# Optimization experiments

Measured on AMD Instinct MI355X. Metric: run time of the kernel, lower is better.

## Reference

```python
import jax, jax.numpy as jnp
import numpy as np

# Dimensions: B batches, E links, T time steps, F flows, rank-r factors, K unrolled iters
B, E, T, F = 16, 256, 4096, 512
RANK = 10
NUM_ITER = 5


def setup_inputs() -> dict:
    key = jax.random.key(0)
    ks = jax.random.split(key, 9)
    Y = jax.random.normal(ks[0], (B, E, T), dtype=jnp.float32)
    R = (jax.random.uniform(ks[1], (B, E, F)) < 0.1).astype(jnp.float32)
    Omega = (jax.random.uniform(ks[2], (B, E, T)) < 0.9).astype(jnp.float32)
    P0 = jax.random.normal(ks[3], (B, E, RANK), dtype=jnp.float32) * 0.1
    Q0 = jax.random.normal(ks[4], (B, T, RANK), dtype=jnp.float32) * 0.1
    # per-iteration learned log-parameters of the unrolled network
    lam_log = jax.random.normal(ks[5], (NUM_ITER,), dtype=jnp.float32) * 0.1 - 1.0
    mu_log = jax.random.normal(ks[6], (NUM_ITER,), dtype=jnp.float32) * 0.1 - 1.0
    nu_log = jax.random.normal(ks[7], (NUM_ITER,), dtype=jnp.float32) * 0.1
    gamma_logit = jax.random.normal(ks[8], (NUM_ITER,), dtype=jnp.float32) * 0.1
    return {"Y": Y, "R": R, "Omega": Omega, "P0": P0, "Q0": Q0,
            "lam_log": lam_log, "mu_log": mu_log, "nu_log": nu_log,
            "gamma_logit": gamma_logit}


def reference(Y, R, Omega, P0, Q0, lam_log, mu_log, nu_log, gamma_logit):
    """Unrolled BSCA: Y ~ X + R @ A + noise on observed entries (Omega mask),
    X relaxed low-rank via factors P (B,E,r), Q (B,T,r); A sparse anomalies (B,F,T).
    Each iteration: rank-r ridge solves for P and Q (left=False -> rhs @ inv(lhs)),
    relaxed X update, soft-thresholded BSCA direction for A + convex-combination step."""
    rank = P0.shape[-1]
    eye = jnp.eye(rank, dtype=Y.dtype)
    X = Omega * Y                     # (B,E,T) init relaxed variable
    A = jnp.zeros((*Y.shape[:-2], R.shape[-1], Y.shape[-1]), dtype=Y.dtype)  # (B,F,T)
    P, Q = P0, Q0
    A_scale = (R * R).mT @ (Omega * Omega)          # (B,F,T)
    noobs = A_scale == 0
    A_scale_safe = A_scale + noobs.astype(Y.dtype)
    for k in range(NUM_ITER):
        lam = jnp.exp(lam_log[k])
        mu = jnp.exp(mu_log[k])
        nu = jnp.exp(nu_log[k])
        gamma = jax.nn.sigmoid(gamma_logit[k])
        regp = lam / nu
        # P update: P = (X @ Q) @ inv(Q^T Q + regp I)   (right solve; lhs symmetric)
        lhsQ = Q.mT @ Q + regp * eye                 # (B,r,r)
        P = jnp.linalg.solve(lhsQ, (X @ Q).mT).mT    # (B,E,r)
        # Q update: Q = (X^T @ P) @ inv(P^T P + regp I)
        lhsP = P.mT @ P + regp * eye
        Q = jnp.linalg.solve(lhsP, (X.mT @ P).mT).mT # (B,T,r)
        # X update (relaxed): X = (Omega*err + nu*P Q^T) / (Omega^2 + nu)
        RA = R @ A                                   # (B,E,T)
        err = Omega * (Y - RA)
        X = (Omega * err + nu * (P @ Q.mT)) / (Omega * Omega + nu)
        # A update: soft-thresholded best-response + convex combination step
        resid = Omega * (Y - X - RA)                 # (B,E,T)
        BA = A + (R.mT @ resid) / A_scale_safe       # (B,F,T)
        A_dir = jnp.sign(BA) * jnp.maximum(jnp.abs(BA) - mu / A_scale_safe, 0.0)
        A_dir = jnp.where(noobs, 0.0, A_dir)
        A = A + gamma * (A_dir - A)
    return A
```

## Files before the change

kernel.cpp:

```cpp
#include <hip/hip_runtime.h>
#include <stdint.h>

#define BB 16
#define EE 256
#define TT 4096
#define FF 512
#define RK 10
#define NIT 5

typedef short bf16x8 __attribute__((ext_vector_type(8)));
typedef float f32x4  __attribute__((ext_vector_type(4)));

__device__ __forceinline__ unsigned short f2bf(float x){
  unsigned int u = __float_as_uint(x);
  unsigned int r = (u + 0x7FFFu + ((u >> 16) & 1u)) >> 16;
  return (unsigned short)r;
}
__device__ __forceinline__ float bf2f(unsigned short s){
  return __uint_as_float(((unsigned int)s) << 16);
}

__device__ __forceinline__ void gld16(const void* g, void* l){
  __builtin_amdgcn_global_load_lds((const __attribute__((address_space(1))) unsigned int*)g,
                                   (__attribute__((address_space(3))) unsigned int*)l,
                                   16, 0, 0);
}

__device__ __forceinline__ int ssw(int r, int s){
  return ((s ^ (r & 3) ^ ((r >> 2) & 3)) << 3);
}


__global__ void k_params(const float* lam_log, const float* mu_log,
                         const float* nu_log, const float* gl, float* prm){
  int k = threadIdx.x;
  if (k < NIT){
    float lam = expf(lam_log[k]);
    float mu  = expf(mu_log[k]);
    float nu  = expf(nu_log[k]);
    float gam = 1.0f/(1.0f+expf(-gl[k]));
    prm[k*8+0]=lam; prm[k*8+1]=mu; prm[k*8+2]=nu; prm[k*8+3]=gam; prm[k*8+4]=lam/nu;
  }
}

__global__ void k_initX(const float4* __restrict__ Y, const float4* __restrict__ Om,
                        float4* __restrict__ X, ushort4* __restrict__ Omb){
  int i = blockIdx.x*256 + threadIdx.x;
  float4 y = Y[i], o = Om[i];
  X[i] = make_float4(y.x*o.x, y.y*o.y, y.z*o.z, y.w*o.w);
  ushort4 ob; ob.x=f2bf(o.x); ob.y=f2bf(o.y); ob.z=f2bf(o.z); ob.w=f2bf(o.w);
  Omb[i] = ob;
}

__global__ void k_ombit(const float* __restrict__ Om, unsigned int* __restrict__ Ombit){
  int tid = threadIdx.x;
  int wv = tid >> 6, lane = tid & 63;
  size_t base = (size_t)blockIdx.x*8192 + (size_t)wv*2048;
  for (int it=0; it<32; ++it){
    float om = Om[base + it*64 + lane];
    unsigned long long m = __ballot(om != 0.0f);
    if (lane==0)  Ombit[(base>>5) + it*2]     = (unsigned int)m;
    if (lane==32) Ombit[(base>>5) + it*2 + 1] = (unsigned int)(m>>32);
  }
}

__global__ void k_qtrans(const float* __restrict__ Q0, float* __restrict__ Qt){
  int idx = blockIdx.x*256 + threadIdx.x;
  int b = idx >> 12, t = idx & (TT-1);
  #pragma unroll
  for (int j=0;j<RK;j++)
    Qt[((size_t)b*RK + j)*TT + t] = Q0[(size_t)idx*RK + j];
}

__global__ void k_rbf(const float4* __restrict__ R, ushort4* __restrict__ Rb){
  int i = blockIdx.x*256 + threadIdx.x;
  float4 v = R[i];
  ushort4 o; o.x=f2bf(v.x); o.y=f2bf(v.y); o.z=f2bf(v.z); o.w=f2bf(v.w);
  Rb[i] = o;
}

__global__ void k_rtransb(const float* __restrict__ Rm, unsigned short* __restrict__ Rbt){
  int f = blockIdx.x, b = blockIdx.y, e = threadIdx.x;
  Rbt[((size_t)b*FF + f)*EE + e] = f2bf(Rm[((size_t)b*EE + e)*FF + f]);
}

__global__ void k_omtrans(const unsigned short* __restrict__ Omb,
                          unsigned short* __restrict__ OmbT){
  __shared__ unsigned short sT[64][66];
  int b  = blockIdx.z;
  int E0 = blockIdx.y*64, T0 = blockIdx.x*64;
  int tid = threadIdx.x;
  int fi = tid >> 4;
  int m  = tid & 15;
  #pragma unroll
  for (int pass=0; pass<4; ++pass){
    int e = pass*16 + fi;
    ushort4 v = *(const ushort4*)(Omb + ((size_t)(b*EE + E0 + e))*TT + T0 + m*4);
    sT[e][m*4+0]=v.x; sT[e][m*4+1]=v.y; sT[e][m*4+2]=v.z; sT[e][m*4+3]=v.w;
  }
  __syncthreads();
  #pragma unroll
  for (int pass=0; pass<4; ++pass){
    int t  = pass*16 + fi;
    int e4 = m*4;
    ushort4 o;
    o.x = sT[e4+0][t]; o.y = sT[e4+1][t];
    o.z = sT[e4+2][t]; o.w = sT[e4+3][t];
    *(ushort4*)(OmbT + ((size_t)b*TT + T0 + t)*EE + E0 + e4) = o;
  }
}


__global__ void k_lhsQ(const float* __restrict__ Qt, const float* __restrict__ prm,
                       float* __restrict__ lhs, int k){
  int p = blockIdx.x, b = blockIdx.y;
  int i = 0, rem = p;
  while (rem >= i+1){ rem -= (i+1); ++i; }
  int j = rem;
  const float* qi = Qt + ((size_t)b*RK + i)*TT;
  const float* qj = Qt + ((size_t)b*RK + j)*TT;
  float a = 0.0f;
  for (int t = threadIdx.x*4; t < TT; t += 1024){
    float4 x = *(const float4*)(qi+t);
    float4 y = *(const float4*)(qj+t);
    a += x.x*y.x + x.y*y.y + x.z*y.z + x.w*y.w;
  }
  __shared__ float red[256];
  red[threadIdx.x] = a; __syncthreads();
  for (int s=128; s>0; s>>=1){
    if (threadIdx.x < s) red[threadIdx.x] += red[threadIdx.x+s];
    __syncthreads();
  }
  if (threadIdx.x==0){
    float v = red[0];
    if (i==j) v += prm[k*8+4];
    lhs[(b*RK+i)*RK + j] = v;
    lhs[(b*RK+j)*RK + i] = v;
  }
}

__global__ void k_lhsP(const float* __restrict__ P, const float* __restrict__ prm,
                       float* __restrict__ lhs, int k){
  int p = blockIdx.x, b = blockIdx.y;
  int i = 0, rem = p;
  while (rem >= i+1){ rem -= (i+1); ++i; }
  int j = rem;
  int e = threadIdx.x;
  const float* pr = P + ((size_t)b*EE + e)*RK;
  float a = pr[i]*pr[j];
  __shared__ float red[256];
  red[threadIdx.x] = a; __syncthreads();
  for (int s=128; s>0; s>>=1){
    if (threadIdx.x < s) red[threadIdx.x] += red[threadIdx.x+s];
    __syncthreads();
  }
  if (threadIdx.x==0){
    float v = red[0];
    if (i==j) v += prm[k*8+4];
    lhs[(b*RK+i)*RK + j] = v;
    lhs[(b*RK+j)*RK + i] = v;
  }
}

__global__ void k_invert(const float* __restrict__ lhs, float* __restrict__ inv){
  int b = blockIdx.x;
  __shared__ float aug[RK][2*RK];
  int tid = threadIdx.x;
  int i = tid / (2*RK), j = tid % (2*RK);
  bool act = tid < RK*2*RK;
  if (act) aug[i][j] = (j < RK) ? lhs[(b*RK+i)*RK + j] : ((j-RK)==i ? 1.0f : 0.0f);
  __syncthreads();
  for (int kk=0; kk<RK; ++kk){
    float pinv = 1.0f / aug[kk][kk];
    __syncthreads();
    if (act && i==kk) aug[i][j] *= pinv;
    __syncthreads();
    float factor = (act && i!=kk) ? aug[i][kk] : 0.0f;
    float pivrow = act ? aug[kk][j] : 0.0f;
    __syncthreads();
    if (act && i!=kk) aug[i][j] -= factor * pivrow;
    __syncthreads();
  }
  if (act && j >= RK) inv[(b*RK+i)*RK + (j-RK)] = aug[i][j];
}

__global__ void k_Pupd(const float* __restrict__ X, const float* __restrict__ Qt,
                       const float* __restrict__ inv, float* __restrict__ P){
  int e = blockIdx.x, b = blockIdx.y;
  const float* xr = X + ((size_t)b*EE + e)*TT;
  const float* qb = Qt + (size_t)b*RK*TT;
  float acc[RK];
  #pragma unroll
  for (int j=0;j<RK;j++) acc[j]=0.0f;
  for (int t = threadIdx.x*4; t < TT; t += 1024){
    float4 x = *(const float4*)(xr+t);
    #pragma unroll
    for (int j=0;j<RK;j++){
      float4 q = *(const float4*)(qb + (size_t)j*TT + t);
      acc[j] += x.x*q.x + x.y*q.y + x.z*q.z + x.w*q.w;
    }
  }
  __shared__ float partial[4][RK];
  int lane = threadIdx.x & 63, wv = threadIdx.x >> 6;
  #pragma unroll
  for (int j=0;j<RK;j++){
    float v = acc[j];
    for (int s=32;s>0;s>>=1) v += __shfl_down(v, s, 64);
    if (lane==0) partial[wv][j] = v;
  }
  __syncthreads();
  if (threadIdx.x < RK){
    int i = threadIdx.x;
    float out = 0.0f;
    #pragma unroll
    for (int j=0;j<RK;j++){
      float xq = partial[0][j]+partial[1][j]+partial[2][j]+partial[3][j];
      out += xq * inv[(b*RK+j)*RK + i];
    }
    P[((size_t)b*EE + e)*RK + i] = out;
  }
}

__global__ void k_Qupd(const float* __restrict__ X, const float* __restrict__ P,
                       const float* __restrict__ inv, float* __restrict__ Qt){
  int b = blockIdx.y;
  int t = blockIdx.x*256 + threadIdx.x;
  __shared__ float sP[EE*RK];
  __shared__ float sInv[RK*RK];
  for (int i=threadIdx.x; i<EE*RK; i+=256) sP[i] = P[(size_t)b*EE*RK + i];
  if (threadIdx.x < RK*RK) sInv[threadIdx.x] = inv[b*RK*RK + threadIdx.x];
  __syncthreads();
  float acc[RK];
  #pragma unroll
  for (int j=0;j<RK;j++) acc[j]=0.0f;
  const float* xb = X + (size_t)b*EE*TT + t;
  for (int e=0;e<EE;e++){
    float x = xb[(size_t)e*TT];
    #pragma unroll
    for (int j=0;j<RK;j++) acc[j] += x * sP[e*RK+j];
  }
  #pragma unroll
  for (int i=0;i<RK;i++){
    float q = 0.0f;
    #pragma unroll
    for (int j=0;j<RK;j++) q += acc[j]*sInv[j*RK+i];
    Qt[((size_t)b*RK + i)*TT + t] = q;
  }
}

__global__ __launch_bounds__(256) void k_gemm1m(
    const unsigned short* __restrict__ Abt, const unsigned short* __restrict__ Rb,
    const float* __restrict__ Y, const unsigned int* __restrict__ Ombit,
    const float* __restrict__ Qt, const float* __restrict__ P,
    const float* __restrict__ prm, float* __restrict__ X,
    unsigned short* __restrict__ residT, int k)
{
  __shared__ __align__(16) unsigned char lds[20480];
  int id = blockIdx.x;
  int b  = id >> 7;
  int e0 = ((id >> 6) & 1) * 128;
  int t0 = (id & 63) * 64;
  int tid  = threadIdx.x;
  int lane = tid & 63, wid = tid >> 6;
  int lr = lane & 15, lg = lane >> 4;
  int wm = wid >> 1, wn = wid & 1;

  f32x4 acc[2][4];
  #pragma unroll
  for (int m=0;m<2;++m)
    #pragma unroll
    for (int n=0;n<4;++n)
      #pragma unroll
      for (int i=0;i<4;++i) acc[m][n][i]=0.0f;

  if (k > 0){
    int swz  = ((lg ^ (lr & 3) ^ ((lr >> 2) & 3)) << 4);
    int aoff = (wm*32 + lr)*64 + swz;
    int boff = 4096 + (wn*64 + lr)*64 + swz;
    int rA = tid >> 2, sA = tid & 3;
    int c0 = tid, c1 = tid + 256;
    int rB0 = c0 >> 2, sB0 = c0 & 3;
    int rB1 = c1 >> 2, sB1 = c1 & 3;
    const unsigned short* gA  = Abt + ((size_t)b*TT + t0 + rA)*FF + ssw(rA,sA);
    const unsigned short* gB0 = Rb  + ((size_t)(b*EE + e0 + rB0))*FF + ssw(rB0,sB0);
    const unsigned short* gB1 = Rb  + ((size_t)(b*EE + e0 + rB1))*FF + ssw(rB1,sB1);
    unsigned char* lA  = lds + tid*16;
    unsigned char* lB0 = lds + 4096 + c0*16;
    unsigned char* lB1 = lds + 4096 + c1*16;

    for (int kk=0; kk<16; ++kk){
      __syncthreads();
      int f0k = kk*32;
      gld16(gA  + f0k, lA);
      gld16(gB0 + f0k, lB0);
      gld16(gB1 + f0k, lB1);
      asm volatile("s_waitcnt vmcnt(0)" ::: "memory");
      __syncthreads();
      bf16x8 af[2], bb[4];
      #pragma unroll
      for (int m=0;m<2;++m) af[m] = *(const bf16x8*)(lds + aoff + m*1024);
      #pragma unroll
      for (int n=0;n<4;++n) bb[n] = *(const bf16x8*)(lds + boff + n*1024);
      #pragma unroll
      for (int m=0;m<2;++m)
        #pragma unroll
        for (int n=0;n<4;++n)
          acc[m][n] = __builtin_amdgcn_mfma_f32_16x16x32_bf16(af[m], bb[n], acc[m][n], 0, 0, 0);
    }
  }

  __syncthreads();
  unsigned short* wbuf = (unsigned short*)(lds + wid*2176);
  float* Pl = (float*)(lds + 12288);
  float* Ql = (float*)(lds + 12288 + 5120);
  for (int idx = tid; idx < 128*RK; idx += 256)
    Pl[idx] = P[((size_t)(b*EE + e0))*RK + idx];
  for (int idx = tid; idx < RK*64; idx += 256){
    int j = idx >> 6, t = idx & 63;
    Ql[idx] = Qt[((size_t)(b*RK + j))*TT + t0 + t];
  }
  __syncthreads();

  float nu = prm[k*8+2];
  #pragma unroll
  for (int m=0;m<2;++m){
    int tq = wm*32 + m*16 + lg*4;
    float4 ql4[RK];
    #pragma unroll
    for (int j=0;j<RK;++j) ql4[j] = *(const float4*)(Ql + j*64 + tq);
    asm volatile("" ::: "memory");
    #pragma unroll
    for (int n=0;n<4;++n){
      int eloc = wn*64 + n*16 + lr;
      const float* pr = Pl + eloc*RK;
      float4 pq = {0,0,0,0};
      #pragma unroll
      for (int j=0;j<RK;++j){
        float pj = pr[j];
        pq.x += pj*ql4[j].x; pq.y += pj*ql4[j].y;
        pq.z += pj*ql4[j].z; pq.w += pj*ql4[j].w;
      }
      f32x4 ra = acc[m][n];
      size_t off = ((size_t)(b*EE + e0 + eloc))*TT + t0 + tq;
      float4 y = *(const float4*)(Y + off);
      unsigned int w = Ombit[off >> 5];
      int sh = (int)(off & 31);
      float4 xo; float rs0, rs1, rs2, rs3;
      {
        float om2 = (w>>(sh+0))&1 ? 1.0f : 0.0f; float d = y.x - ra[0];
        xo.x = (om2*d + nu*pq.x)/(om2 + nu); rs0 = om2*(y.x - xo.x - ra[0]);
      }{
        float om2 = (w>>(sh+1))&1 ? 1.0f : 0.0f; float d = y.y - ra[1];
        xo.y = (om2*d + nu*pq.y)/(om2 + nu); rs1 = om2*(y.y - xo.y - ra[1]);
      }{
        float om2 = (w>>(sh+2))&1 ? 1.0f : 0.0f; float d = y.z - ra[2];
        xo.z = (om2*d + nu*pq.z)/(om2 + nu); rs2 = om2*(y.z - xo.z - ra[2]);
      }{
        float om2 = (w>>(sh+3))&1 ? 1.0f : 0.0f; float d = y.w - ra[3];
        xo.w = (om2*d + nu*pq.w)/(om2 + nu); rs3 = om2*(y.w - xo.w - ra[3]);
      }
      *(float4*)(X + off) = xo;
      int wc = n*16 + lr;
      wbuf[(lg*4+0)*68 + wc] = f2bf(rs0);
      wbuf[(lg*4+1)*68 + wc] = f2bf(rs1);
      wbuf[(lg*4+2)*68 + wc] = f2bf(rs2);
      wbuf[(lg*4+3)*68 + wc] = f2bf(rs3);
    }
    asm volatile("" ::: "memory");
    #pragma unroll
    for (int j2=0;j2<4;++j2){
      int row = j2*4 + lg;
      int c4  = lr*4;
      ushort4 vv = *(const ushort4*)(wbuf + row*68 + c4);
      *(ushort4*)(residT + ((size_t)b*TT + t0 + wm*32 + m*16 + row)*EE + e0 + wn*64 + c4) = vv;
    }
    asm volatile("" ::: "memory");
  }
}

__device__ __forceinline__ float aupd(float a, float g, unsigned short asu,
                                      float mu, float gamma){
  float as = bf2f(asu);
  bool no = (as == 0.0f);
  float rs = 1.0f / (no ? 1.0f : as);
  float ba = a + g*rs;
  float ad = copysignf(fmaxf(fabsf(ba) - mu*rs, 0.0f), ba);
  if (no) ad = 0.0f;
  return a + gamma*(ad - a);
}

__global__ __launch_bounds__(256) void k_gemm2m(
    const unsigned short* __restrict__ residT, const unsigned short* __restrict__ Rbt,
    const unsigned short* __restrict__ As, const float* __restrict__ prm,
    float* __restrict__ A, unsigned short* __restrict__ Abt, int k)
{
  __shared__ __align__(16) unsigned char lds[12288];
  int id = blockIdx.x;
  int b  = id >> 8;
  int f0 = ((id >> 5) & 7) * 64;
  int t0 = (id & 31) * 128;
  int tid  = threadIdx.x;
  int lane = tid & 63, wid = tid >> 6;
  int lr = lane & 15, lg = lane >> 4;
  int wm = wid >> 1, wn = wid & 1;

  f32x4 acc[4][2];
  #pragma unroll
  for (int m=0;m<4;++m)
    #pragma unroll
    for (int n=0;n<2;++n)
      #pragma unroll
      for (int i=0;i<4;++i) acc[m][n][i]=0.0f;

  int swz  = ((lg ^ (lr & 3) ^ ((lr >> 2) & 3)) << 4);
  int aoff = (wm*64 + lr)*64 + swz;
  int boff = 8192 + (wn*32 + lr)*64 + swz;
  int c0 = tid, c1 = tid + 256;
  int r0 = c0 >> 2, s0 = c0 & 3;
  int r1 = c1 >> 2, s1 = c1 & 3;
  int rB = tid >> 2, sB = tid & 3;
  const unsigned short* gA0 = residT + ((size_t)b*TT + t0 + r0)*EE + ssw(r0,s0);
  const unsigned short* gA1 = residT + ((size_t)b*TT + t0 + r1)*EE + ssw(r1,s1);
  const unsigned short* gB  = Rbt    + ((size_t)(b*FF + f0 + rB))*EE + ssw(rB,sB);
  unsigned char* lA0 = lds + c0*16;
  unsigned char* lA1 = lds + c1*16;
  unsigned char* lB  = lds + 8192 + tid*16;

  for (int kk=0; kk<8; ++kk){
    __syncthreads();
    int eoff = kk*32;
    gld16(gA0 + eoff, lA0);
    gld16(gA1 + eoff, lA1);
    gld16(gB  + eoff, lB);
    asm volatile("s_waitcnt vmcnt(0)" ::: "memory");
    __syncthreads();
    bf16x8 af[4], bb[2];
    #pragma unroll
    for (int m=0;m<4;++m) af[m] = *(const bf16x8*)(lds + aoff + m*1024);
    #pragma unroll
    for (int n=0;n<2;++n) bb[n] = *(const bf16x8*)(lds + boff + n*1024);
    #pragma unroll
    for (int m=0;m<4;++m)
      #pragma unroll
      for (int n=0;n<2;++n)
        acc[m][n] = __builtin_amdgcn_mfma_f32_16x16x32_bf16(af[m], bb[n], acc[m][n], 0, 0, 0);
  }

  __syncthreads();
  unsigned short* wbuf = (unsigned short*)(lds + wid*1152);
  float mu = prm[k*8+1], gamma = prm[k*8+3];
  bool emit = (k < NIT-1);
  #pragma unroll
  for (int m=0;m<4;++m){
    int tq = wm*64 + m*16 + lg*4;
    #pragma unroll
    for (int n=0;n<2;++n){
      int floc = wn*32 + n*16 + lr;
      size_t off = ((size_t)(b*FF + f0 + floc))*TT + t0 + tq;
      float4 a = *(const float4*)(A + off);
      ushort4 as4 = *(const ushort4*)(As + off);
      f32x4 g = acc[m][n];
      float4 an;
      an.x = aupd(a.x, g[0], as4.x, mu, gamma);
      an.y = aupd(a.y, g[1], as4.y, mu, gamma);
      an.z = aupd(a.z, g[2], as4.z, mu, gamma);
      an.w = aupd(a.w, g[3], as4.w, mu, gamma);
      *(float4*)(A + off) = an;
      if (emit){
        int wc = n*16 + lr;
        wbuf[(lg*4+0)*36 + wc] = f2bf(an.x);
        wbuf[(lg*4+1)*36 + wc] = f2bf(an.y);
        wbuf[(lg*4+2)*36 + wc] = f2bf(an.z);
        wbuf[(lg*4+3)*36 + wc] = f2bf(an.w);
      }
    }
    asm volatile("" ::: "memory");
    if (emit){
      #pragma unroll
      for (int j2=0;j2<2;++j2){
        int row = j2*8 + (lane >> 3);
        int c4  = (lane & 7)*4;
        ushort4 vv = *(const ushort4*)(wbuf + row*36 + c4);
        *(ushort4*)(Abt + ((size_t)b*TT + t0 + wm*64 + m*16 + row)*FF + f0 + wn*32 + c4) = vv;
      }
    }
    asm volatile("" ::: "memory");
  }
}

__global__ __launch_bounds__(256) void k_ascalem(
    const unsigned short* __restrict__ OmbT, const unsigned short* __restrict__ Rbt,
    unsigned short* __restrict__ As)
{
  __shared__ __align__(16) unsigned char lds[16384];
  int id = blockIdx.x;
  int b  = id >> 7;
  int f0 = ((id >> 5) & 3) * 128;
  int t0 = (id & 31) * 128;
  int tid  = threadIdx.x;
  int lane = tid & 63, wid = tid >> 6;
  int lr = lane & 15, lg = lane >> 4;
  int wm = wid >> 1, wn = wid & 1;

  f32x4 acc[4][4];
  #pragma unroll
  for (int m=0;m<4;++m)
    #pragma unroll
    for (int n=0;n<4;++n)
      #pragma unroll
      for (int i=0;i<4;++i) acc[m][n][i]=0.0f;

  int swz  = ((lg ^ (lr & 3) ^ ((lr >> 2) & 3)) << 4);
  int aoff = (wm*64 + lr)*64 + swz;
  int boff = 8192 + (wn*64 + lr)*64 + swz;
  int c0 = tid, c1 = tid + 256;
  int r0 = c0 >> 2, s0 = c0 & 3;
  int r1 = c1 >> 2, s1 = c1 & 3;
  const unsigned short* gA0 = OmbT + ((size_t)b*TT + t0 + r0)*EE + ssw(r0,s0);
  const unsigned short* gA1 = OmbT + ((size_t)b*TT + t0 + r1)*EE + ssw(r1,s1);
  const unsigned short* gB0 = Rbt  + ((size_t)(b*FF + f0 + r0))*EE + ssw(r0,s0);
  const unsigned short* gB1 = Rbt  + ((size_t)(b*FF + f0 + r1))*EE + ssw(r1,s1);
  unsigned char* lA0 = lds + c0*16;
  unsigned char* lA1 = lds + c1*16;
  unsigned char* lB0 = lds + 8192 + c0*16;
  unsigned char* lB1 = lds + 8192 + c1*16;

  for (int kk=0; kk<8; ++kk){
    __syncthreads();
    int eoff = kk*32;
    gld16(gA0 + eoff, lA0);
    gld16(gA1 + eoff, lA1);
    gld16(gB0 + eoff, lB0);
    gld16(gB1 + eoff, lB1);
    asm volatile("s_waitcnt vmcnt(0)" ::: "memory");
    __syncthreads();
    bf16x8 af[4], bb[4];
    #pragma unroll
    for (int m=0;m<4;++m) af[m] = *(const bf16x8*)(lds + aoff + m*1024);
    #pragma unroll
    for (int n=0;n<4;++n) bb[n] = *(const bf16x8*)(lds + boff + n*1024);
    #pragma unroll
    for (int m=0;m<4;++m)
      #pragma unroll
      for (int n=0;n<4;++n)
        acc[m][n] = __builtin_amdgcn_mfma_f32_16x16x32_bf16(af[m], bb[n], acc[m][n], 0, 0, 0);
  }

  #pragma unroll
  for (int m=0;m<4;++m){
    int tq = wm*64 + m*16 + lg*4;
    #pragma unroll
    for (int n=0;n<4;++n){
      int floc = wn*64 + n*16 + lr;
      size_t off = ((size_t)(b*FF + f0 + floc))*TT + t0 + tq;
      ushort4 o;
      o.x = f2bf(acc[m][n][0]); o.y = f2bf(acc[m][n][1]);
      o.z = f2bf(acc[m][n][2]); o.w = f2bf(acc[m][n][3]);
      *(ushort4*)(As + off) = o;
    }
  }
}


extern "C" void kernel_launch(void* const* d_in, const int* in_sizes, int n_in,
                              void* d_out, int out_size, void* d_ws, size_t ws_size,
                              hipStream_t stream){
  const float* Y   = (const float*)d_in[0];
  const float* Rm  = (const float*)d_in[1];
  const float* Om  = (const float*)d_in[2];
  const float* P0  = (const float*)d_in[3];
  const float* Q0  = (const float*)d_in[4];
  const float* lam = (const float*)d_in[5];
  const float* mu  = (const float*)d_in[6];
  const float* nu  = (const float*)d_in[7];
  const float* gl  = (const float*)d_in[8];
  float* A = (float*)d_out;

  char* ws = (char*)d_ws;
  const size_t X_OFF    = 0;
  const size_t REST_OFF = X_OFF    + (size_t)BB*EE*TT*4;
  const size_t OMB_OFF  = REST_OFF + (size_t)BB*TT*EE*2;
  const size_t AS_OFF   = OMB_OFF  + (size_t)BB*EE*TT*2;
  const size_t QT_OFF   = AS_OFF   + (size_t)BB*FF*TT*2;
  const size_t P_OFF    = QT_OFF   + (size_t)BB*RK*TT*4;
  const size_t LHS_OFF  = P_OFF    + (size_t)BB*EE*RK*4;
  const size_t INV_OFF  = LHS_OFF  + (size_t)BB*RK*RK*4;
  const size_t PRM_OFF  = INV_OFF  + (size_t)BB*RK*RK*4;
  const size_t RB_OFF   = PRM_OFF  + 4096;
  const size_t RBT_OFF  = RB_OFF   + (size_t)BB*EE*FF*2;
  const size_t OMBT_OFF = RBT_OFF  + (size_t)BB*FF*EE*2;
  const size_t ABT_OFF  = OMBT_OFF + (size_t)BB*TT*EE*2;
  const size_t OBIT_OFF = ABT_OFF  + (size_t)BB*TT*FF*2;

  float* X    = (float*)(ws + X_OFF);
  unsigned short* residT = (unsigned short*)(ws + REST_OFF);
  unsigned short* Omb    = (unsigned short*)(ws + OMB_OFF);
  unsigned short* As     = (unsigned short*)(ws + AS_OFF);
  float* Qt   = (float*)(ws + QT_OFF);
  float* P    = (float*)(ws + P_OFF);
  float* lhs  = (float*)(ws + LHS_OFF);
  float* inv  = (float*)(ws + INV_OFF);
  float* prm  = (float*)(ws + PRM_OFF);
  unsigned short* Rb    = (unsigned short*)(ws + RB_OFF);
  unsigned short* Rbt   = (unsigned short*)(ws + RBT_OFF);
  unsigned short* OmbT  = (unsigned short*)(ws + OMBT_OFF);
  unsigned short* Abt   = (unsigned short*)(ws + ABT_OFF);
  unsigned int*   Ombit = (unsigned int*)(ws + OBIT_OFF);

  (void)P0; (void)in_sizes; (void)n_in; (void)ws_size;

  hipMemsetAsync(d_out, 0, (size_t)out_size*sizeof(float), stream);
  k_params<<<1, 64, 0, stream>>>(lam, mu, nu, gl, prm);
  k_initX<<<BB*EE*TT/4/256, 256, 0, stream>>>((const float4*)Y, (const float4*)Om,
                                              (float4*)X, (ushort4*)Omb);
  k_ombit<<<BB*EE*TT/8192, 256, 0, stream>>>(Om, Ombit);
  k_qtrans<<<BB*TT/256, 256, 0, stream>>>(Q0, Qt);
  k_rbf<<<BB*EE*FF/4/256, 256, 0, stream>>>((const float4*)Rm, (ushort4*)Rb);
  k_rtransb<<<dim3(FF, BB), 256, 0, stream>>>(Rm, Rbt);
  k_omtrans<<<dim3(TT/64, EE/64, BB), 256, 0, stream>>>(Omb, OmbT);
  k_ascalem<<<2048, 256, 0, stream>>>(OmbT, Rbt, As);

  for (int k=0; k<NIT; ++k){
    k_lhsQ  <<<dim3(55, BB), 256, 0, stream>>>(Qt, prm, lhs, k);
    k_invert<<<BB, 256, 0, stream>>>(lhs, inv);
    k_Pupd  <<<dim3(EE, BB), 256, 0, stream>>>(X, Qt, inv, P);
    k_lhsP  <<<dim3(55, BB), 256, 0, stream>>>(P, prm, lhs, k);
    k_invert<<<BB, 256, 0, stream>>>(lhs, inv);
    k_Qupd  <<<dim3(TT/256, BB), 256, 0, stream>>>(X, P, inv, Qt);
    k_gemm1m<<<2048, 256, 0, stream>>>(Abt, Rb, Y, Ombit, Qt, P, prm, X, residT, k);
    k_gemm2m<<<4096, 256, 0, stream>>>(residT, Rbt, As, prm, A, Abt, k);
  }
}
```

Before: 1.806 ms.

## Store X in bf16 and double-buffer LDS loads in the three MFMA GEMMs

The relaxed variable X is now stored as bf16 instead of fp32, which halves its read and write traffic in the P/Q updates and in the gemm1 epilogue. Separately, the three MFMA GEMM kernels now use two LDS buffers and issue the next k-slice's global-to-LDS loads before computing the current one, overlapping memory latency with MFMA work. The cost is lower precision in X feeding the P/Q solves, more LDS per block (which may reduce occupancy), and an extra barrier per k-iteration.

```diff
diff --git a/kernel.cpp b/kernel.cpp
--- a/kernel.cpp
+++ b/kernel.cpp
@@ -44,10 +44,11 @@
 }
 
 __global__ void k_initX(const float4* __restrict__ Y, const float4* __restrict__ Om,
-                        float4* __restrict__ X, ushort4* __restrict__ Omb){
+                        ushort4* __restrict__ Xb, ushort4* __restrict__ Omb){
   int i = blockIdx.x*256 + threadIdx.x;
   float4 y = Y[i], o = Om[i];
-  X[i] = make_float4(y.x*o.x, y.y*o.y, y.z*o.z, y.w*o.w);
+  ushort4 xb; xb.x=f2bf(y.x*o.x); xb.y=f2bf(y.y*o.y); xb.z=f2bf(y.z*o.z); xb.w=f2bf(y.w*o.w);
+  Xb[i] = xb;
   ushort4 ob; ob.x=f2bf(o.x); ob.y=f2bf(o.y); ob.z=f2bf(o.z); ob.w=f2bf(o.w);
   Omb[i] = ob;
 }
@@ -184,20 +185,25 @@
   if (act && j >= RK) inv[(b*RK+i)*RK + (j-RK)] = aug[i][j];
 }
 
-__global__ void k_Pupd(const float* __restrict__ X, const float* __restrict__ Qt,
+__global__ void k_Pupd(const unsigned short* __restrict__ Xb, const float* __restrict__ Qt,
                        const float* __restrict__ inv, float* __restrict__ P){
   int e = blockIdx.x, b = blockIdx.y;
-  const float* xr = X + ((size_t)b*EE + e)*TT;
+  const unsigned short* xr = Xb + ((size_t)b*EE + e)*TT;
   const float* qb = Qt + (size_t)b*RK*TT;
   float acc[RK];
   #pragma unroll
   for (int j=0;j<RK;j++) acc[j]=0.0f;
-  for (int t = threadIdx.x*4; t < TT; t += 1024){
-    float4 x = *(const float4*)(xr+t);
+  for (int t = threadIdx.x*8; t < TT; t += 2048){
+    bf16x8 xv = *(const bf16x8*)(xr+t);
+    float xf[8];
+    #pragma unroll
+    for (int i=0;i<8;++i) xf[i] = bf2f((unsigned short)xv[i]);
     #pragma unroll
     for (int j=0;j<RK;j++){
-      float4 q = *(const float4*)(qb + (size_t)j*TT + t);
-      acc[j] += x.x*q.x + x.y*q.y + x.z*q.z + x.w*q.w;
+      float4 qa = *(const float4*)(qb + (size_t)j*TT + t);
+      float4 qc = *(const float4*)(qb + (size_t)j*TT + t + 4);
+      acc[j] += xf[0]*qa.x + xf[1]*qa.y + xf[2]*qa.z + xf[3]*qa.w
+              + xf[4]*qc.x + xf[5]*qc.y + xf[6]*qc.z + xf[7]*qc.w;
     }
   }
   __shared__ float partial[4][RK];
@@ -221,7 +227,7 @@
   }
 }
 
-__global__ void k_Qupd(const float* __restrict__ X, const float* __restrict__ P,
+__global__ void k_Qupd(const unsigned short* __restrict__ Xb, const float* __restrict__ P,
                        const float* __restrict__ inv, float* __restrict__ Qt){
   int b = blockIdx.y;
   int t = blockIdx.x*256 + threadIdx.x;
@@ -233,9 +239,9 @@
   float acc[RK];
   #pragma unroll
   for (int j=0;j<RK;j++) acc[j]=0.0f;
-  const float* xb = X + (size_t)b*EE*TT + t;
+  const unsigned short* xb = Xb + (size_t)b*EE*TT + t;
   for (int e=0;e<EE;e++){
-    float x = xb[(size_t)e*TT];
+    float x = bf2f(xb[(size_t)e*TT]);
     #pragma unroll
     for (int j=0;j<RK;j++) acc[j] += x * sP[e*RK+j];
   }
@@ -252,10 +258,10 @@
     const unsigned short* __restrict__ Abt, const unsigned short* __restrict__ Rb,
     const float* __restrict__ Y, const unsigned int* __restrict__ Ombit,
     const float* __restrict__ Qt, const float* __restrict__ P,
-    const float* __restrict__ prm, float* __restrict__ X,
+    const float* __restrict__ prm, unsigned short* __restrict__ Xb,
     unsigned short* __restrict__ residT, int k)
 {
-  __shared__ __align__(16) unsigned char lds[20480];
+  __shared__ __align__(16) unsigned char lds[32768];
   int id = blockIdx.x;
   int b  = id >> 7;
   int e0 = ((id >> 6) & 1) * 128;
@@ -284,35 +290,42 @@
     const unsigned short* gA  = Abt + ((size_t)b*TT + t0 + rA)*FF + ssw(rA,sA);
     const unsigned short* gB0 = Rb  + ((size_t)(b*EE + e0 + rB0))*FF + ssw(rB0,sB0);
     const unsigned short* gB1 = Rb  + ((size_t)(b*EE + e0 + rB1))*FF + ssw(rB1,sB1);
-    unsigned char* lA  = lds + tid*16;
-    unsigned char* lB0 = lds + 4096 + c0*16;
-    unsigned char* lB1 = lds + 4096 + c1*16;
-
+
+    gld16(gA,  lds + tid*16);
+    gld16(gB0, lds + 4096 + c0*16);
+    gld16(gB1, lds + 4096 + c1*16);
+    #pragma unroll
     for (int kk=0; kk<16; ++kk){
-      __syncthreads();
-      int f0k = kk*32;
-      gld16(gA  + f0k, lA);
-      gld16(gB0 + f0k, lB0);
-      gld16(gB1 + f0k, lB1);
-      asm volatile("s_waitcnt vmcnt(0)" ::: "memory");
+      int cur = (kk&1)*12288;
+      if (kk < 15){
+        int nxt = ((kk+1)&1)*12288;
+        int f0k = (kk+1)*32;
+        gld16(gA  + f0k, lds + nxt + tid*16);
+        gld16(gB0 + f0k, lds + nxt + 4096 + c0*16);
+        gld16(gB1 + f0k, lds + nxt + 4096 + c1*16);
+        asm volatile("s_waitcnt vmcnt(3)" ::: "memory");
+      } else {
+        asm volatile("s_waitcnt vmcnt(0)" ::: "memory");
+      }
       __syncthreads();
       bf16x8 af[2], bb[4];
       #pragma unroll
-      for (int m=0;m<2;++m) af[m] = *(const bf16x8*)(lds + aoff + m*1024);
-      #pragma unroll
-      for (int n=0;n<4;++n) bb[n] = *(const bf16x8*)(lds + boff + n*1024);
+      for (int m=0;m<2;++m) af[m] = *(const bf16x8*)(lds + cur + aoff + m*1024);
+      #pragma unroll
+      for (int n=0;n<4;++n) bb[n] = *(const bf16x8*)(lds + cur + boff + n*1024);
       #pragma unroll
       for (int m=0;m<2;++m)
         #pragma unroll
         for (int n=0;n<4;++n)
           acc[m][n] = __builtin_amdgcn_mfma_f32_16x16x32_bf16(af[m], bb[n], acc[m][n], 0, 0, 0);
+      __syncthreads();
     }
   }
 
   __syncthreads();
   unsigned short* wbuf = (unsigned short*)(lds + wid*2176);
-  float* Pl = (float*)(lds + 12288);
-  float* Ql = (float*)(lds + 12288 + 5120);
+  float* Pl = (float*)(lds + 24576);
+  float* Ql = (float*)(lds + 24576 + 5120);
   for (int idx = tid; idx < 128*RK; idx += 256)
     Pl[idx] = P[((size_t)(b*EE + e0))*RK + idx];
   for (int idx = tid; idx < RK*64; idx += 256){
@@ -345,21 +358,21 @@
       float4 y = *(const float4*)(Y + off);
       unsigned int w = Ombit[off >> 5];
       int sh = (int)(off & 31);
-      float4 xo; float rs0, rs1, rs2, rs3;
+      float rs0, rs1, rs2, rs3; ushort4 xb4;
       {
         float om2 = (w>>(sh+0))&1 ? 1.0f : 0.0f; float d = y.x - ra[0];
-        xo.x = (om2*d + nu*pq.x)/(om2 + nu); rs0 = om2*(y.x - xo.x - ra[0]);
+        float x = (om2*d + nu*pq.x)/(om2 + nu); rs0 = om2*(y.x - x - ra[0]); xb4.x = f2bf(x);
       }{
         float om2 = (w>>(sh+1))&1 ? 1.0f : 0.0f; float d = y.y - ra[1];
-        xo.y = (om2*d + nu*pq.y)/(om2 + nu); rs1 = om2*(y.y - xo.y - ra[1]);
+        float x = (om2*d + nu*pq.y)/(om2 + nu); rs1 = om2*(y.y - x - ra[1]); xb4.y = f2bf(x);
       }{
         float om2 = (w>>(sh+2))&1 ? 1.0f : 0.0f; float d = y.z - ra[2];
-        xo.z = (om2*d + nu*pq.z)/(om2 + nu); rs2 = om2*(y.z - xo.z - ra[2]);
+        float x = (om2*d + nu*pq.z)/(om2 + nu); rs2 = om2*(y.z - x - ra[2]); xb4.z = f2bf(x);
       }{
         float om2 = (w>>(sh+3))&1 ? 1.0f : 0.0f; float d = y.w - ra[3];
-        xo.w = (om2*d + nu*pq.w)/(om2 + nu); rs3 = om2*(y.w - xo.w - ra[3]);
+        float x = (om2*d + nu*pq.w)/(om2 + nu); rs3 = om2*(y.w - x - ra[3]); xb4.w = f2bf(x);
       }
-      *(float4*)(X + off) = xo;
+      *(ushort4*)(Xb + off) = xb4;
       int wc = n*16 + lr;
       wbuf[(lg*4+0)*68 + wc] = f2bf(rs0);
       wbuf[(lg*4+1)*68 + wc] = f2bf(rs1);
@@ -394,7 +407,7 @@
     const unsigned short* __restrict__ As, const float* __restrict__ prm,
     float* __restrict__ A, unsigned short* __restrict__ Abt, int k)
 {
-  __shared__ __align__(16) unsigned char lds[12288];
+  __shared__ __align__(16) unsigned char lds[24576];
   int id = blockIdx.x;
   int b  = id >> 8;
   int f0 = ((id >> 5) & 7) * 64;
@@ -422,28 +435,35 @@
   const unsigned short* gA0 = residT + ((size_t)b*TT + t0 + r0)*EE + ssw(r0,s0);
   const unsigned short* gA1 = residT + ((size_t)b*TT + t0 + r1)*EE + ssw(r1,s1);
   const unsigned short* gB  = Rbt    + ((size_t)(b*FF + f0 + rB))*EE + ssw(rB,sB);
-  unsigned char* lA0 = lds + c0*16;
-  unsigned char* lA1 = lds + c1*16;
-  unsigned char* lB  = lds + 8192 + tid*16;
-
+
+  gld16(gA0, lds + c0*16);
+  gld16(gA1, lds + c1*16);
+  gld16(gB,  lds + 8192 + tid*16);
+  #pragma unroll
   for (int kk=0; kk<8; ++kk){
-    __syncthreads();
-    int eoff = kk*32;
-    gld16(gA0 + eoff, lA0);
-    gld16(gA1 + eoff, lA1);
-    gld16(gB  + eoff, lB);
-    asm volatile("s_waitcnt vmcnt(0)" ::: "memory");
+    int cur = (kk&1)*12288;
+    if (kk < 7){
+      int nxt = ((kk+1)&1)*12288;
+      int eoff = (kk+1)*32;
+      gld16(gA0 + eoff, lds + nxt + c0*16);
+      gld16(gA1 + eoff, lds + nxt + c1*16);
+      gld16(gB  + eoff, lds + nxt + 8192 + tid*16);
+      asm volatile("s_waitcnt vmcnt(3)" ::: "memory");
+    } else {
+      asm volatile("s_waitcnt vmcnt(0)" ::: "memory");
+    }
     __syncthreads();
     bf16x8 af[4], bb[2];
     #pragma unroll
-    for (int m=0;m<4;++m) af[m] = *(const bf16x8*)(lds + aoff + m*1024);
-    #pragma unroll
-    for (int n=0;n<2;++n) bb[n] = *(const bf16x8*)(lds + boff + n*1024);
+    for (int m=0;m<4;++m) af[m] = *(const bf16x8*)(lds + cur + aoff + m*1024);
+    #pragma unroll
+    for (int n=0;n<2;++n) bb[n] = *(const bf16x8*)(lds + cur + boff + n*1024);
     #pragma unroll
     for (int m=0;m<4;++m)
       #pragma unroll
       for (int n=0;n<2;++n)
         acc[m][n] = __builtin_amdgcn_mfma_f32_16x16x32_bf16(af[m], bb[n], acc[m][n], 0, 0, 0);
+    __syncthreads();
   }
 
   __syncthreads();
@@ -492,7 +512,7 @@
     const unsigned short* __restrict__ OmbT, const unsigned short* __restrict__ Rbt,
     unsigned short* __restrict__ As)
 {
-  __shared__ __align__(16) unsigned char lds[16384];
+  __shared__ __align__(16) unsigned char lds[32768];
   int id = blockIdx.x;
   int b  = id >> 7;
   int f0 = ((id >> 5) & 3) * 128;
@@ -520,30 +540,37 @@
   const unsigned short* gA1 = OmbT + ((size_t)b*TT + t0 + r1)*EE + ssw(r1,s1);
   const unsigned short* gB0 = Rbt  + ((size_t)(b*FF + f0 + r0))*EE + ssw(r0,s0);
   const unsigned short* gB1 = Rbt  + ((size_t)(b*FF + f0 + r1))*EE + ssw(r1,s1);
-  unsigned char* lA0 = lds + c0*16;
-  unsigned char* lA1 = lds + c1*16;
-  unsigned char* lB0 = lds + 8192 + c0*16;
-  unsigned char* lB1 = lds + 8192 + c1*16;
-
+
+  gld16(gA0, lds + c0*16);
+  gld16(gA1, lds + c1*16);
+  gld16(gB0, lds + 8192 + c0*16);
+  gld16(gB1, lds + 8192 + c1*16);
+  #pragma unroll
   for (int kk=0; kk<8; ++kk){
-    __syncthreads();
-    int eoff = kk*32;
-    gld16(gA0 + eoff, lA0);
-    gld16(gA1 + eoff, lA1);
-    gld16(gB0 + eoff, lB0);
-    gld16(gB1 + eoff, lB1);
-    asm volatile("s_waitcnt vmcnt(0)" ::: "memory");
+    int cur = (kk&1)*16384;
+    if (kk < 7){
+      int nxt = ((kk+1)&1)*16384;
+      int eoff = (kk+1)*32;
+      gld16(gA0 + eoff, lds + nxt + c0*16);
+      gld16(gA1 + eoff, lds + nxt + c1*16);
+      gld16(gB0 + eoff, lds + nxt + 8192 + c0*16);
+      gld16(gB1 + eoff, lds + nxt + 8192 + c1*16);
+      asm volatile("s_waitcnt vmcnt(4)" ::: "memory");
+    } else {
+      asm volatile("s_waitcnt vmcnt(0)" ::: "memory");
+    }
     __syncthreads();
     bf16x8 af[4], bb[4];
     #pragma unroll
-    for (int m=0;m<4;++m) af[m] = *(const bf16x8*)(lds + aoff + m*1024);
-    #pragma unroll
-    for (int n=0;n<4;++n) bb[n] = *(const bf16x8*)(lds + boff + n*1024);
+    for (int m=0;m<4;++m) af[m] = *(const bf16x8*)(lds + cur + aoff + m*1024);
+    #pragma unroll
+    for (int n=0;n<4;++n) bb[n] = *(const bf16x8*)(lds + cur + boff + n*1024);
     #pragma unroll
     for (int m=0;m<4;++m)
       #pragma unroll
       for (int n=0;n<4;++n)
         acc[m][n] = __builtin_amdgcn_mfma_f32_16x16x32_bf16(af[m], bb[n], acc[m][n], 0, 0, 0);
+    __syncthreads();
   }
 
   #pragma unroll
@@ -592,7 +619,7 @@
   const size_t ABT_OFF  = OMBT_OFF + (size_t)BB*TT*EE*2;
   const size_t OBIT_OFF = ABT_OFF  + (size_t)BB*TT*FF*2;
 
-  float* X    = (float*)(ws + X_OFF);
+  unsigned short* Xb     = (unsigned short*)(ws + X_OFF);
   unsigned short* residT = (unsigned short*)(ws + REST_OFF);
   unsigned short* Omb    = (unsigned short*)(ws + OMB_OFF);
   unsigned short* As     = (unsigned short*)(ws + AS_OFF);
@@ -612,7 +639,7 @@
   hipMemsetAsync(d_out, 0, (size_t)out_size*sizeof(float), stream);
   k_params<<<1, 64, 0, stream>>>(lam, mu, nu, gl, prm);
   k_initX<<<BB*EE*TT/4/256, 256, 0, stream>>>((const float4*)Y, (const float4*)Om,
-                                              (float4*)X, (ushort4*)Omb);
+                                              (ushort4*)Xb, (ushort4*)Omb);
   k_ombit<<<BB*EE*TT/8192, 256, 0, stream>>>(Om, Ombit);
   k_qtrans<<<BB*TT/256, 256, 0, stream>>>(Q0, Qt);
   k_rbf<<<BB*EE*FF/4/256, 256, 0, stream>>>((const float4*)Rm, (ushort4*)Rb);
@@ -623,11 +650,11 @@
   for (int k=0; k<NIT; ++k){
     k_lhsQ  <<<dim3(55, BB), 256, 0, stream>>>(Qt, prm, lhs, k);
     k_invert<<<BB, 256, 0, stream>>>(lhs, inv);
-    k_Pupd  <<<dim3(EE, BB), 256, 0, stream>>>(X, Qt, inv, P);
+    k_Pupd  <<<dim3(EE, BB), 256, 0, stream>>>(Xb, Qt, inv, P);
     k_lhsP  <<<dim3(55, BB), 256, 0, stream>>>(P, prm, lhs, k);
     k_invert<<<BB, 256, 0, stream>>>(lhs, inv);
-    k_Qupd  <<<dim3(TT/256, BB), 256, 0, stream>>>(X, P, inv, Qt);
-    k_gemm1m<<<2048, 256, 0, stream>>>(Abt, Rb, Y, Ombit, Qt, P, prm, X, residT, k);
+    k_Qupd  <<<dim3(TT/256, BB), 256, 0, stream>>>(Xb, P, inv, Qt);
+    k_gemm1m<<<2048, 256, 0, stream>>>(Abt, Rb, Y, Ombit, Qt, P, prm, Xb, residT, k);
     k_gemm2m<<<4096, 256, 0, stream>>>(residT, Rbt, As, prm, A, Abt, k);
   }
 }
```

Result: slower. 1.848 ms (+2.3%).
